# Performance work log

Hardware: AMD Instinct MI355X
Metric: run time of the kernel (lower is better)

The kernel has to match this reference:

```python
import jax, jax.numpy as jnp
import numpy as np

V, E, A, U, ENC = 10000, 512, 512, 512, 2048  # vocab, embed, attn, lstm, encoder units
B, P, S = 64, 196, 22  # batch, num_pixels, max sequence length


def setup_inputs() -> dict:
    key = jax.random.key(0)
    ks = jax.random.split(key, 16)
    init = lambda k, sh: jax.random.normal(k, sh, jnp.float32) * 0.02
    seq_lens = jax.random.randint(ks[2], (B,), 2, S + 1).at[0].set(S)  # ensure max len present
    return {
        "encoder_output": jax.random.normal(ks[0], (B, P, ENC), jnp.float32),
        "sequences": jax.random.randint(ks[1], (B, S), 0, V),
        "sequence_lengths": seq_lens,
        "emb_table": init(ks[3], (V, E)),
        "W_att_enc": init(ks[4], (ENC, A)), "b_att_enc": jnp.zeros((A,), jnp.float32),
        "W_att_gen": init(ks[5], (U, A)), "b_att_gen": jnp.zeros((A,), jnp.float32),
        "W_att_full": init(ks[6], (A, 1)), "b_att_full": jnp.zeros((1,), jnp.float32),
        "W_x": init(ks[7], (E + ENC, 4 * U)), "W_h": init(ks[8], (U, 4 * U)),
        "b_lstm": jnp.zeros((4 * U,), jnp.float32),
        "W_init_m": init(ks[9], (ENC, U)), "b_init_m": jnp.zeros((U,), jnp.float32),
        "W_init_c": init(ks[10], (ENC, U)), "b_init_c": jnp.zeros((U,), jnp.float32),
        "W_beta": init(ks[11], (U, ENC)), "b_beta": jnp.zeros((ENC,), jnp.float32),
        "W_out": init(ks[12], (U, V)), "b_out": jnp.zeros((V,), jnp.float32),
    }


def reference(encoder_output, sequences, sequence_lengths, emb_table,
              W_att_enc, b_att_enc, W_att_gen, b_att_gen, W_att_full, b_att_full,
              W_x, W_h, b_lstm, W_init_m, b_init_m, W_init_c, b_init_c,
              W_beta, b_beta, W_out, b_out):
    # Sort batch by descending caption length (as in the TF code)
    order = jnp.argsort(-sequence_lengths)
    enc = encoder_output[order]            # [B,P,ENC]
    seqs = sequences[order]                # [B,S]
    iter_lens = sequence_lengths[order] - 1  # [B]
    T = sequences.shape[1] - 1

    emb = emb_table[seqs]                  # [B,S,E]
    mean_enc = enc.mean(axis=1)            # [B,ENC]
    h = mean_enc @ W_init_m + b_init_m     # keras LSTMCell states[0] (== memory_state)
    c = mean_enc @ W_init_c + b_init_c     # keras LSTMCell states[1] (== carry_state)
    att1 = enc @ W_att_enc + b_att_enc     # [B,P,A], precomputed (constant across steps)

    def step(carry, xt):
        h, c, = carry
        emb_t, t = xt                      # emb_t: [B,E]
        mask = (t < iter_lens)[:, None]    # active rows at step t (sorted desc -> prefix)
        # attention over pixels, conditioned on carry state c
        att2 = c @ W_att_gen + b_att_gen                       # [B,A]
        e = (jax.nn.relu(att1 + att2[:, None, :]) @ W_att_full)[..., 0] + b_att_full[0]  # [B,P]
        alpha = jax.nn.softmax(e, axis=1)                      # [B,P]
        awe = jnp.einsum('bpe,bp->be', enc, alpha)             # [B,ENC]
        beta = jax.nn.sigmoid(c @ W_beta + b_beta)             # [B,ENC]
        awe = awe * beta
        # LSTM cell step (keras gate order: i, f, g, o)
        x = jnp.concatenate([emb_t, awe], axis=1)              # [B,E+ENC]
        z = x @ W_x + h @ W_h + b_lstm                         # [B,4U]
        i, f, g, o = jnp.split(z, 4, axis=1)
        c_new = jax.nn.sigmoid(f) * c + jax.nn.sigmoid(i) * jnp.tanh(g)
        h_new = jax.nn.sigmoid(o) * jnp.tanh(c_new)
        h2 = jnp.where(mask, h_new, h)
        c2 = jnp.where(mask, c_new, c)
        pred = jax.nn.softmax(c2 @ W_out + b_out, axis=1)      # prediction from carry state
        pred = jnp.where(mask, pred, 0.0)
        alpha = jnp.where(mask, alpha, 0.0)
        return (h2, c2), (pred, alpha)

    xs = (jnp.swapaxes(emb[:, :T], 0, 1), jnp.arange(T))
    _, (preds, alphas) = jax.lax.scan(step, (h, c), xs)
    predictions = jnp.swapaxes(preds, 0, 1)        # [B,T,V]
    attention_alphas = jnp.swapaxes(alphas, 0, 1)  # [B,T,P]
    return predictions, attention_alphas, seqs, iter_lens, order
```

## Files before the change

### kernel.cpp

```cpp
#include <hip/hip_runtime.h>
#include <math.h>

#define BB 64
#define PP 196
#define SS 22
#define TT 21
#define VV 10000
#define EE 512
#define AA 512
#define UU 512
#define EC 2048

#define OUT_PRED  0
#define OUT_ALPHA (BB*TT*VV)
#define OUT_SEQ   (OUT_ALPHA + BB*TT*PP)
#define OUT_ILEN  (OUT_SEQ + BB*SS)
#define OUT_ORDER (OUT_ILEN + BB)

__device__ __forceinline__ float sigm(float x) { return 1.0f / (1.0f + expf(-x)); }

__global__ void k_sort(const int* __restrict__ lens, const int* __restrict__ seqs,
                       int* __restrict__ order, int* __restrict__ ilens,
                       float* __restrict__ out)
{
    __shared__ int ord_s[BB];
    int i = threadIdx.x;
    int li = lens[i];
    int rank = 0;
    for (int j = 0; j < BB; ++j) {
        int lj = lens[j];
        rank += (lj > li) || (lj == li && j < i);
    }
    ord_s[rank] = i;
    __syncthreads();
    int o = ord_s[i];
    order[i] = o;
    int il = lens[o] - 1;
    ilens[i] = il;
    for (int s = 0; s < SS; ++s)
        out[OUT_SEQ + i * SS + s] = (float)seqs[o * SS + s];
    out[OUT_ILEN + i] = (float)il;
    out[OUT_ORDER + i] = (float)o;
}

__global__ void k_rowoff(const int* __restrict__ order, const int* __restrict__ seqs,
                         int* __restrict__ roff1, int* __restrict__ roff2)
{
    int idx = blockIdx.x * 256 + threadIdx.x;
    if (idx < BB * PP) {
        int b = idx / PP, p = idx % PP;
        roff1[idx] = order[b] * (PP * EC) + p * EC;
    }
    if (idx < BB * TT) {
        int b = idx / TT, t = idx % TT;
        int tok = seqs[order[b] * SS + t];
        roff2[idx] = tok * EE;
    }
}

__global__ __launch_bounds__(256) void k_mean(const float* __restrict__ enc,
                                              const int* __restrict__ order,
                                              float* __restrict__ meanE)
{
    int idx = blockIdx.x * 256 + threadIdx.x;
    int b = idx >> 11, e = idx & 2047;
    const float* base = enc + (size_t)order[b] * (PP * EC) + e;
    float s = 0.f;
    for (int p = 0; p < PP; ++p) s += base[p * EC];
    meanE[idx] = s * (1.0f / PP);
}

__global__ __launch_bounds__(256) void k_gemm_tile(
    const float* __restrict__ Abase, const int* __restrict__ roff,
    const float* __restrict__ W, const float* __restrict__ bias,
    float* __restrict__ C, int M, int N, int K)
{
    __shared__ float As[16][128];
    __shared__ float Bs[16][128];
    int nwg = gridDim.x, bid = blockIdx.x;
    int q = nwg >> 3, r = nwg & 7;
    int x = bid & 7, y = bid >> 3;
    int lbid = (x < r ? x * (q + 1) : r * (q + 1) + (x - r) * q) + y;
    int ntn = N >> 7;
    int mt = lbid / ntn, nt = lbid % ntn;
    int tid = threadIdx.x;

    int arow = tid >> 1, akq = (tid & 1) * 8;
    int am = mt * 128 + arow; if (am > M - 1) am = M - 1;
    const float* aptr = Abase + (size_t)roff[am] + akq;
    int bkr = tid >> 5, bc4 = (tid & 31) * 4;
    const float* bptr = W + (size_t)bkr * N + nt * 128 + bc4;

    float4 a0 = *(const float4*)(aptr);
    float4 a1 = *(const float4*)(aptr + 4);
    float4 b0 = *(const float4*)(bptr);
    float4 b1 = *(const float4*)(bptr + (size_t)8 * N);

    int tr = tid >> 4, tc = tid & 15;
    float acc[8][8] = {};

    for (int k0 = 0; k0 < K; k0 += 16) {
        float* ac = &As[akq][arow];
        ac[0]   = a0.x; ac[128] = a0.y; ac[256] = a0.z; ac[384] = a0.w;
        ac[512] = a1.x; ac[640] = a1.y; ac[768] = a1.z; ac[896] = a1.w;
        *(float4*)&Bs[bkr][bc4] = b0;
        *(float4*)&Bs[bkr + 8][bc4] = b1;
        __syncthreads();
        if (k0 + 16 < K) {
            a0 = *(const float4*)(aptr + k0 + 16);
            a1 = *(const float4*)(aptr + k0 + 20);
            b0 = *(const float4*)(bptr + (size_t)(k0 + 16) * N);
            b1 = *(const float4*)(bptr + (size_t)(k0 + 24) * N);
        }
        #pragma unroll
        for (int kk = 0; kk < 16; ++kk) {
            float4 aL = *(float4*)&As[kk][tr * 4];
            float4 aH = *(float4*)&As[kk][tr * 4 + 64];
            float4 bL = *(float4*)&Bs[kk][tc * 4];
            float4 bH = *(float4*)&Bs[kk][tc * 4 + 64];
            float av[8] = {aL.x, aL.y, aL.z, aL.w, aH.x, aH.y, aH.z, aH.w};
            float bv[8] = {bL.x, bL.y, bL.z, bL.w, bH.x, bH.y, bH.z, bH.w};
            #pragma unroll
            for (int i = 0; i < 8; ++i)
                #pragma unroll
                for (int j = 0; j < 8; ++j)
                    acc[i][j] += av[i] * bv[j];
        }
        __syncthreads();
    }
    float4 bL = make_float4(0.f, 0.f, 0.f, 0.f), bH = bL;
    if (bias) {
        bL = *(const float4*)&bias[nt * 128 + tc * 4];
        bH = *(const float4*)&bias[nt * 128 + tc * 4 + 64];
    }
    #pragma unroll
    for (int ih = 0; ih < 2; ++ih)
        #pragma unroll
        for (int i2 = 0; i2 < 4; ++i2) {
            int i = ih * 4 + i2;
            int m = mt * 128 + ih * 64 + tr * 4 + i2;
            if (m < M) {
                float4 lo, hi;
                lo.x = acc[i][0] + bL.x; lo.y = acc[i][1] + bL.y;
                lo.z = acc[i][2] + bL.z; lo.w = acc[i][3] + bL.w;
                hi.x = acc[i][4] + bH.x; hi.y = acc[i][5] + bH.y;
                hi.z = acc[i][6] + bH.z; hi.w = acc[i][7] + bH.w;
                *(float4*)&C[(size_t)m * N + nt * 128 + tc * 4] = lo;
                *(float4*)&C[(size_t)m * N + nt * 128 + tc * 4 + 64] = hi;
            }
        }
}

__global__ __launch_bounds__(256) void k_initmc(
    const float* __restrict__ meanE, const float* __restrict__ Wim,
    const float* __restrict__ bim, const float* __restrict__ Wic,
    const float* __restrict__ bic, float* __restrict__ hB, float* __restrict__ cB)
{
    __shared__ float xs[16 * 512];
    int ry = blockIdx.y, ct = blockIdx.x;
    const float* W   = blockIdx.z ? Wic : Wim;
    const float* bia = blockIdx.z ? bic : bim;
    float* out       = blockIdx.z ? cB : hB;
    int ng = threadIdx.x & 31, rg = threadIdx.x >> 5;
    int col = ct * 128 + ng * 4;
    float acc[2][4] = {};
    for (int kc = 0; kc < 4; ++kc) {
        __syncthreads();
        for (int it = 0; it < 8; ++it) {
            int i4 = (it * 256 + threadIdx.x) * 4;
            int rr = i4 >> 9, k = i4 & 511;
            *(float4*)&xs[i4] =
                *(const float4*)&meanE[(size_t)(ry * 16 + rr) * EC + kc * 512 + k];
        }
        __syncthreads();
        const float* wp = W + (size_t)(kc * 512) * 512 + col;
        #pragma unroll 8
        for (int k = 0; k < 512; ++k) {
            float4 w = *(const float4*)(wp + (size_t)k * 512);
            float x0 = xs[(rg * 2) * 512 + k], x1 = xs[(rg * 2 + 1) * 512 + k];
            acc[0][0] += x0 * w.x; acc[0][1] += x0 * w.y; acc[0][2] += x0 * w.z; acc[0][3] += x0 * w.w;
            acc[1][0] += x1 * w.x; acc[1][1] += x1 * w.y; acc[1][2] += x1 * w.z; acc[1][3] += x1 * w.w;
        }
    }
    int r0 = ry * 16 + rg * 2;
    float4 bv = *(const float4*)&bia[col];
    float4 o0, o1;
    o0.x = acc[0][0] + bv.x; o0.y = acc[0][1] + bv.y; o0.z = acc[0][2] + bv.z; o0.w = acc[0][3] + bv.w;
    o1.x = acc[1][0] + bv.x; o1.y = acc[1][1] + bv.y; o1.z = acc[1][2] + bv.z; o1.w = acc[1][3] + bv.w;
    *(float4*)&out[(size_t)r0 * 512 + col] = o0;
    *(float4*)&out[(size_t)(r0 + 1) * 512 + col] = o1;
}

__device__ __forceinline__ void mm64(
    float* __restrict__ xs,
    const float* __restrict__ x, int ldx, int kbase,
    const float* __restrict__ W, int ldw, int col0, int collim,
    float* __restrict__ dst, int ldd,
    int tcheck, const int* __restrict__ ilens)
{
    int tid = threadIdx.x;
    #pragma unroll
    for (int it = 0; it < 8; ++it) {
        int f4 = it * 256 + tid;
        int r = f4 >> 5, kf = (f4 & 31) * 4;
        *(float4*)&xs[r * 132 + kf] = *(const float4*)&x[(size_t)r * ldx + kbase + kf];
    }
    __syncthreads();
    int ng = tid & 31, rg = tid >> 5;
    int col = col0 + ng * 4;
    if (col + 4 > collim) return;
    float acc[8][4] = {};
    const float* wp = W + (size_t)kbase * ldw + col;
    #pragma unroll 4
    for (int k = 0; k < 128; ++k) {
        float4 w = *(const float4*)(wp + (size_t)k * ldw);
        #pragma unroll
        for (int i = 0; i < 8; ++i) {
            float xv = xs[(rg * 8 + i) * 132 + k];
            acc[i][0] += xv * w.x; acc[i][1] += xv * w.y;
            acc[i][2] += xv * w.z; acc[i][3] += xv * w.w;
        }
    }
    #pragma unroll
    for (int i = 0; i < 8; ++i) {
        int r = rg * 8 + i;
        if (tcheck < ilens[r])
            *(float4*)&dst[(size_t)r * ldd + col] = *(float4*)&acc[i][0];
    }
}

__device__ __forceinline__ void ab_part(
    float* xs, int b2, const float* cB, const float* Wag, const float* Wb,
    float* att2P, float* betaP, int tcheck, const int* ilens)
{
    int ct = b2 >> 2, kz = b2 & 3;
    if (ct < 4)
        mm64(xs, cB, 512, kz * 128, Wag, 512, ct * 128, 1 << 30,
             att2P + (size_t)kz * (BB * AA), 512, tcheck, ilens);
    else
        mm64(xs, cB, 512, kz * 128, Wb, 2048, (ct - 4) * 128, 1 << 30,
             betaP + (size_t)kz * (BB * EC), 2048, tcheck, ilens);
}

__global__ __launch_bounds__(256) void k_ab0(
    const float* __restrict__ cB, const float* __restrict__ Wag,
    const float* __restrict__ Wb, float* __restrict__ att2P,
    float* __restrict__ betaP, const int* __restrict__ ilens)
{
    __shared__ float xs[64 * 132];
    ab_part(xs, blockIdx.x, cB, Wag, Wb, att2P, betaP, 0, ilens);
}

__global__ __launch_bounds__(256) void k_fused1(
    const float* __restrict__ cB, const float* __restrict__ Wo,
    const float* __restrict__ Wag, const float* __restrict__ Wb,
    float* __restrict__ logitP, float* __restrict__ att2P,
    float* __restrict__ betaP, const int* __restrict__ ilens, int t)
{
    __shared__ float xs[64 * 132];
    int bid = blockIdx.x;
    if (bid < 316) {
        int ct = bid >> 2, kz = bid & 3;
        mm64(xs, cB, 512, kz * 128, Wo, VV, ct * 128, VV,
             logitP + (size_t)kz * (BB * VV), VV, t, ilens);
    } else if (t + 1 < TT) {
        ab_part(xs, bid - 316, cB, Wag, Wb, att2P, betaP, t + 1, ilens);
    }
}

__global__ __launch_bounds__(256) void k_zg(
    const float* __restrict__ aweB, const float* __restrict__ hB,
    const float* __restrict__ Wx2, const float* __restrict__ Wh,
    float* __restrict__ zP, const int* __restrict__ ilens, int t)
{
    __shared__ float xs[64 * 132];
    int ct = blockIdx.x, kz = blockIdx.y;
    if (kz < 16)
        mm64(xs, aweB, 2048, kz * 128, Wx2, 2048, ct * 128, 1 << 30,
             zP + (size_t)kz * (BB * EC), 2048, t, ilens);
    else
        mm64(xs, hB, 512, (kz - 16) * 128, Wh, 2048, ct * 128, 1 << 30,
             zP + (size_t)kz * (BB * EC), 2048, t, ilens);
}

__global__ __launch_bounds__(512) void k_scorepred(
    const float* __restrict__ att1, const float* __restrict__ att2P,
    const float* __restrict__ bgen, const float* __restrict__ Wf,
    const float* __restrict__ logitP, const float* __restrict__ bout,
    const int* __restrict__ ilens, float* __restrict__ alphaS,
    float* __restrict__ out, int t)
{
    int tid = threadIdx.x;
    if (blockIdx.x < 64) {
        int b = blockIdx.x;
        if (t >= TT || t >= ilens[b]) return;
        __shared__ float att2g[AA], wfs[AA], es[PP], red[512];
        att2g[tid] = att2P[b * AA + tid] + att2P[BB * AA + b * AA + tid]
                   + att2P[2 * BB * AA + b * AA + tid] + att2P[3 * BB * AA + b * AA + tid]
                   + bgen[tid];
        wfs[tid] = Wf[tid];
        __syncthreads();
        int wv = tid >> 6, lane = tid & 63;
        int a0 = lane * 8;
        float4 g0 = *(float4*)&att2g[a0], g1 = *(float4*)&att2g[a0 + 4];
        float4 w0 = *(float4*)&wfs[a0],  w1 = *(float4*)&wfs[a0 + 4];
        for (int p = wv; p < PP; p += 8) {
            const float4* A1 = (const float4*)(att1 + ((size_t)b * PP + p) * AA + a0);
            float4 x0 = A1[0], x1 = A1[1];
            float acc = fmaxf(x0.x + g0.x, 0.f) * w0.x + fmaxf(x0.y + g0.y, 0.f) * w0.y
                      + fmaxf(x0.z + g0.z, 0.f) * w0.z + fmaxf(x0.w + g0.w, 0.f) * w0.w
                      + fmaxf(x1.x + g1.x, 0.f) * w1.x + fmaxf(x1.y + g1.y, 0.f) * w1.y
                      + fmaxf(x1.z + g1.z, 0.f) * w1.z + fmaxf(x1.w + g1.w, 0.f) * w1.w;
            #pragma unroll
            for (int s = 32; s; s >>= 1) acc += __shfl_down(acc, s);
            if (lane == 0) es[p] = acc;
        }
        __syncthreads();
        float ev = (tid < PP) ? es[tid] : -1e30f;
        red[tid] = ev; __syncthreads();
        for (int s = 256; s >= 1; s >>= 1) {
            if (tid < s) red[tid] = fmaxf(red[tid], red[tid + s]);
            __syncthreads();
        }
        float mx = red[0]; __syncthreads();
        float ex = (tid < PP) ? expf(ev - mx) : 0.f;
        red[tid] = ex; __syncthreads();
        for (int s = 256; s >= 1; s >>= 1) {
            if (tid < s) red[tid] += red[tid + s];
            __syncthreads();
        }
        float inv = 1.0f / red[0];
        if (tid < PP) {
            float al = ex * inv;
            alphaS[b * PP + tid] = al;
            out[OUT_ALPHA + ((size_t)b * TT + t) * PP + tid] = al;
        }
    } else {
        int b = blockIdx.x - 64;
        int tp = t - 1;
        if (tp < 0 || tp >= ilens[b]) return;
        __shared__ float red8[8];
        int lane = tid & 63, wv = tid >> 6;
        const float* lb = logitP + (size_t)b * VV;
        float v[20];
        #pragma unroll
        for (int i = 0; i < 20; ++i) {
            int idx = tid + i * 512;
            if (idx < VV) {
                v[i] = lb[idx] + lb[BB * VV + idx] + lb[2 * BB * VV + idx]
                     + lb[3 * BB * VV + idx] + bout[idx];
            } else v[i] = -1e30f;
        }
        float mx = v[0];
        #pragma unroll
        for (int i = 1; i < 20; ++i) mx = fmaxf(mx, v[i]);
        #pragma unroll
        for (int s = 32; s; s >>= 1) mx = fmaxf(mx, __shfl_xor(mx, s));
        if (lane == 0) red8[wv] = mx;
        __syncthreads();
        if (tid == 0) {
            float m2 = red8[0];
            for (int i = 1; i < 8; ++i) m2 = fmaxf(m2, red8[i]);
            red8[0] = m2;
        }
        __syncthreads();
        mx = red8[0];
        __syncthreads();
        float sm = 0.f;
        #pragma unroll
        for (int i = 0; i < 20; ++i) {
            int idx = tid + i * 512;
            float e = (idx < VV) ? expf(v[i] - mx) : 0.f;
            v[i] = e; sm += e;
        }
        #pragma unroll
        for (int s = 32; s; s >>= 1) sm += __shfl_xor(sm, s);
        if (lane == 0) red8[wv] = sm;
        __syncthreads();
        if (tid == 0) {
            float s2 = 0.f;
            for (int i = 0; i < 8; ++i) s2 += red8[i];
            red8[0] = s2;
        }
        __syncthreads();
        float inv = 1.0f / red8[0];
        float* po = out + OUT_PRED + ((size_t)b * TT + tp) * VV;
        #pragma unroll
        for (int i = 0; i < 20; ++i) {
            int idx = tid + i * 512;
            if (idx < VV) po[idx] = v[i] * inv;
        }
    }
}

__global__ __launch_bounds__(256) void k_awe(
    const float* __restrict__ alphaS, const float* __restrict__ enc,
    const int* __restrict__ order, const int* __restrict__ ilens,
    const float* __restrict__ betaP, const float* __restrict__ bbeta,
    float* __restrict__ awe, int t)
{
    int b = blockIdx.y;
    if (t >= ilens[b]) return;
    int chunk = blockIdx.x, tid = threadIdx.x;
    __shared__ float al[PP];
    if (tid < PP) al[tid] = alphaS[b * PP + tid];
    __syncthreads();
    int e = chunk * 256 + tid;
    const float* ebase = enc + (size_t)order[b] * (PP * EC) + e;
    float s = 0.f;
    #pragma unroll 4
    for (int p = 0; p < PP; ++p) s += al[p] * ebase[(size_t)p * EC];
    float br = bbeta[e] + betaP[b * EC + e] + betaP[BB * EC + b * EC + e]
             + betaP[2 * BB * EC + b * EC + e] + betaP[3 * BB * EC + b * EC + e];
    awe[b * EC + e] = s * sigm(br);
}

__global__ __launch_bounds__(256) void k_gates(
    const float* __restrict__ zP, const float* __restrict__ zemb,
    const float* __restrict__ blstm, float* __restrict__ h, float* __restrict__ c,
    const int* __restrict__ ilens, int t)
{
    int idx = blockIdx.x * 256 + threadIdx.x;
    int b = idx >> 9, u = idx & 511;
    if (t >= ilens[b]) return;
    const float* ze = zemb + ((size_t)b * TT + t) * EC;
    float g[4];
    #pragma unroll
    for (int j = 0; j < 4; ++j) {
        float s = ze[u + j * 512] + blstm[u + j * 512];
        #pragma unroll
        for (int kc = 0; kc < 20; ++kc)
            s += zP[(size_t)kc * (BB * EC) + b * EC + u + j * 512];
        g[j] = s;
    }
    float cold = c[idx];
    float cn = sigm(g[1]) * cold + sigm(g[0]) * tanhf(g[2]);
    float hn = sigm(g[3]) * tanhf(cn);
    c[idx] = cn; h[idx] = hn;
}

extern "C" void kernel_launch(void* const* d_in, const int* in_sizes, int n_in,
                              void* d_out, int out_size, void* d_ws, size_t ws_size,
                              hipStream_t stream)
{
    (void)in_sizes; (void)n_in; (void)out_size; (void)ws_size;
    const float* enc  = (const float*)d_in[0];
    const int*   seqs = (const int*)d_in[1];
    const int*   lens = (const int*)d_in[2];
    const float* embT = (const float*)d_in[3];
    const float* W_ae = (const float*)d_in[4];
    const float* b_ae = (const float*)d_in[5];
    const float* W_ag = (const float*)d_in[6];
    const float* b_ag = (const float*)d_in[7];
    const float* W_af = (const float*)d_in[8];
    const float* W_x  = (const float*)d_in[10];
    const float* W_h  = (const float*)d_in[11];
    const float* b_l  = (const float*)d_in[12];
    const float* W_im = (const float*)d_in[13];
    const float* b_im = (const float*)d_in[14];
    const float* W_ic = (const float*)d_in[15];
    const float* b_ic = (const float*)d_in[16];
    const float* W_b  = (const float*)d_in[17];
    const float* b_b  = (const float*)d_in[18];
    const float* W_o  = (const float*)d_in[19];
    const float* b_o  = (const float*)d_in[20];
    float* out = (float*)d_out;

    float* ws     = (float*)d_ws;
    float* att1   = ws;
    float* zemb   = att1 + 6422528;
    float* alphaS = zemb + 2752512;
    float* aweB   = alphaS + 12544;
    float* att2P  = aweB + 131072;
    float* betaP  = att2P + 131072;
    float* hB     = betaP + 524288;
    float* cB     = hB + 32768;
    float* zlP    = cB + 32768;
    int* order = (int*)(zlP + 2621440);
    int* ilens = order + 64;
    int* roff1 = ilens + 64;
    int* roff2 = roff1 + 12544;
    float* meanE  = att2P;
    float* zP     = zlP;
    float* logitP = zlP;

    hipMemsetAsync(out, 0, (size_t)OUT_SEQ * 4, stream);

    k_sort<<<1, 64, 0, stream>>>(lens, seqs, order, ilens, out);
    k_rowoff<<<49, 256, 0, stream>>>(order, seqs, roff1, roff2);
    k_mean<<<512, 256, 0, stream>>>(enc, order, meanE);
    k_initmc<<<dim3(4, 4, 2), 256, 0, stream>>>(meanE, W_im, b_im, W_ic, b_ic, hB, cB);

    k_gemm_tile<<<98 * 4, 256, 0, stream>>>(enc, roff1, W_ae, b_ae, att1, 12544, 512, 2048);
    k_gemm_tile<<<11 * 16, 256, 0, stream>>>(embT, roff2, W_x, nullptr, zemb, 1344, 2048, 512);

    k_ab0<<<80, 256, 0, stream>>>(cB, W_ag, W_b, att2P, betaP, ilens);

    const float* Wx2 = W_x + (size_t)512 * 2048;
    for (int t = 0; t < TT; ++t) {
        k_scorepred<<<128, 512, 0, stream>>>(
            att1, att2P, b_ag, W_af, logitP, b_o, ilens, alphaS, out, t);
        k_awe<<<dim3(8, 64), 256, 0, stream>>>(
            alphaS, enc, order, ilens, betaP, b_b, aweB, t);
        k_zg<<<dim3(16, 20), 256, 0, stream>>>(aweB, hB, Wx2, W_h, zP, ilens, t);
        k_gates<<<128, 256, 0, stream>>>(zP, zemb, b_l, hB, cB, ilens, t);
        k_fused1<<<396, 256, 0, stream>>>(
            cB, W_o, W_ag, W_b, logitP, att2P, betaP, ilens, t);
    }
    k_scorepred<<<128, 512, 0, stream>>>(
        att1, att2P, b_ag, W_af, logitP, b_o, ilens, alphaS, out, TT);
}
```

Measured before the change: 2.616 ms.

## Fuse per-timestep decoder kernels into one persistent kernel with grid barriers

```diff
diff --git a/kernel.cpp b/kernel.cpp
--- a/kernel.cpp
+++ b/kernel.cpp
@@ -10,6 +10,7 @@
 #define AA 512
 #define UU 512
 #define EC 2048
+#define NBLK 512u
 
 #define OUT_PRED  0
 #define OUT_ALPHA (BB*TT*VV)
@@ -191,7 +192,27 @@
     *(float4*)&out[(size_t)(r0 + 1) * 512 + col] = o1;
 }
 
-__device__ __forceinline__ void mm64(
+__device__ __forceinline__ void gridbar(unsigned* __restrict__ bar,
+                                        unsigned* __restrict__ gen)
+{
+    __syncthreads();
+    if (threadIdx.x == 0) {
+        __threadfence();
+        unsigned g = atomicAdd(gen, 0u);
+        if (atomicAdd(bar, 1u) == NBLK - 1u) {
+            atomicExch(bar, 0u);
+            atomicAdd(gen, 1u);
+        } else {
+            unsigned spins = 0;
+            while (atomicAdd(gen, 0u) == g && ++spins < (1u << 22))
+                __builtin_amdgcn_s_sleep(1);
+        }
+        __threadfence();
+    }
+    __syncthreads();
+}
+
+__device__ __forceinline__ void mm64p(
     float* __restrict__ xs,
     const float* __restrict__ x, int ldx, int kbase,
     const float* __restrict__ W, int ldw, int col0, int collim,
@@ -208,25 +229,27 @@
     __syncthreads();
     int ng = tid & 31, rg = tid >> 5;
     int col = col0 + ng * 4;
-    if (col + 4 > collim) return;
-    float acc[8][4] = {};
-    const float* wp = W + (size_t)kbase * ldw + col;
-    #pragma unroll 4
-    for (int k = 0; k < 128; ++k) {
-        float4 w = *(const float4*)(wp + (size_t)k * ldw);
+    if (col + 4 <= collim) {
+        float acc[8][4] = {};
+        const float* wp = W + (size_t)kbase * ldw + col;
+        #pragma unroll 4
+        for (int k = 0; k < 128; ++k) {
+            float4 w = *(const float4*)(wp + (size_t)k * ldw);
+            #pragma unroll
+            for (int i = 0; i < 8; ++i) {
+                float xv = xs[(rg * 8 + i) * 132 + k];
+                acc[i][0] += xv * w.x; acc[i][1] += xv * w.y;
+                acc[i][2] += xv * w.z; acc[i][3] += xv * w.w;
+            }
+        }
         #pragma unroll
         for (int i = 0; i < 8; ++i) {
-            float xv = xs[(rg * 8 + i) * 132 + k];
-            acc[i][0] += xv * w.x; acc[i][1] += xv * w.y;
-            acc[i][2] += xv * w.z; acc[i][3] += xv * w.w;
-        }
-    }
-    #pragma unroll
-    for (int i = 0; i < 8; ++i) {
-        int r = rg * 8 + i;
-        if (tcheck < ilens[r])
-            *(float4*)&dst[(size_t)r * ldd + col] = *(float4*)&acc[i][0];
-    }
+            int r = rg * 8 + i;
+            if (tcheck < ilens[r])
+                *(float4*)&dst[(size_t)r * ldd + col] = *(float4*)&acc[i][0];
+        }
+    }
+    __syncthreads();
 }
 
 __device__ __forceinline__ void ab_part(
@@ -235,208 +258,230 @@
 {
     int ct = b2 >> 2, kz = b2 & 3;
     if (ct < 4)
-        mm64(xs, cB, 512, kz * 128, Wag, 512, ct * 128, 1 << 30,
-             att2P + (size_t)kz * (BB * AA), 512, tcheck, ilens);
+        mm64p(xs, cB, 512, kz * 128, Wag, 512, ct * 128, 1 << 30,
+              att2P + (size_t)kz * (BB * AA), 512, tcheck, ilens);
     else
-        mm64(xs, cB, 512, kz * 128, Wb, 2048, (ct - 4) * 128, 1 << 30,
-             betaP + (size_t)kz * (BB * EC), 2048, tcheck, ilens);
-}
-
-__global__ __launch_bounds__(256) void k_ab0(
-    const float* __restrict__ cB, const float* __restrict__ Wag,
-    const float* __restrict__ Wb, float* __restrict__ att2P,
-    float* __restrict__ betaP, const int* __restrict__ ilens)
-{
-    __shared__ float xs[64 * 132];
-    ab_part(xs, blockIdx.x, cB, Wag, Wb, att2P, betaP, 0, ilens);
-}
-
-__global__ __launch_bounds__(256) void k_fused1(
-    const float* __restrict__ cB, const float* __restrict__ Wo,
-    const float* __restrict__ Wag, const float* __restrict__ Wb,
-    float* __restrict__ logitP, float* __restrict__ att2P,
-    float* __restrict__ betaP, const int* __restrict__ ilens, int t)
-{
-    __shared__ float xs[64 * 132];
+        mm64p(xs, cB, 512, kz * 128, Wb, 2048, (ct - 4) * 128, 1 << 30,
+              betaP + (size_t)kz * (BB * EC), 2048, tcheck, ilens);
+}
+
+__device__ void score_part(
+    float* smem, int b, const float* __restrict__ att1,
+    const float* __restrict__ att2P, const float* __restrict__ bgen,
+    const float* __restrict__ Wf, const int* __restrict__ ilens,
+    float* __restrict__ alphaS, float* __restrict__ out, int t)
+{
+    if (t >= ilens[b]) return;
+    float* att2g = smem;
+    float* wfs   = smem + 512;
+    float* es    = smem + 1024;
+    float* red   = smem + 1232;
+    int tid = threadIdx.x;
+    for (int i = tid; i < AA; i += 256) {
+        float s = bgen[i];
+        #pragma unroll
+        for (int kz = 0; kz < 4; ++kz) s += att2P[(size_t)kz * BB * AA + b * AA + i];
+        att2g[i] = s;
+        wfs[i] = Wf[i];
+    }
+    __syncthreads();
+    int wv = tid >> 6, lane = tid & 63, a0 = lane * 8;
+    float4 g0 = *(float4*)&att2g[a0], g1 = *(float4*)&att2g[a0 + 4];
+    float4 w0 = *(float4*)&wfs[a0],  w1 = *(float4*)&wfs[a0 + 4];
+    for (int p = wv; p < PP; p += 4) {
+        const float4* A1 = (const float4*)(att1 + ((size_t)b * PP + p) * AA + a0);
+        float4 x0 = A1[0], x1 = A1[1];
+        float acc = fmaxf(x0.x + g0.x, 0.f) * w0.x + fmaxf(x0.y + g0.y, 0.f) * w0.y
+                  + fmaxf(x0.z + g0.z, 0.f) * w0.z + fmaxf(x0.w + g0.w, 0.f) * w0.w
+                  + fmaxf(x1.x + g1.x, 0.f) * w1.x + fmaxf(x1.y + g1.y, 0.f) * w1.y
+                  + fmaxf(x1.z + g1.z, 0.f) * w1.z + fmaxf(x1.w + g1.w, 0.f) * w1.w;
+        #pragma unroll
+        for (int s = 32; s; s >>= 1) acc += __shfl_down(acc, s);
+        if (lane == 0) es[p] = acc;
+    }
+    __syncthreads();
+    float ev = (tid < PP) ? es[tid] : -1e30f;
+    red[tid] = ev; __syncthreads();
+    for (int s = 128; s >= 1; s >>= 1) {
+        if (tid < s) red[tid] = fmaxf(red[tid], red[tid + s]);
+        __syncthreads();
+    }
+    float mx = red[0]; __syncthreads();
+    float ex = (tid < PP) ? expf(ev - mx) : 0.f;
+    red[tid] = ex; __syncthreads();
+    for (int s = 128; s >= 1; s >>= 1) {
+        if (tid < s) red[tid] += red[tid + s];
+        __syncthreads();
+    }
+    float inv = 1.0f / red[0];
+    if (tid < PP) {
+        float a = ex * inv;
+        alphaS[b * PP + tid] = a;
+        out[OUT_ALPHA + ((size_t)b * TT + t) * PP + tid] = a;
+    }
+}
+
+__device__ void awe_part(
+    float* smem, int bid, const float* __restrict__ alphaS,
+    const float* __restrict__ enc, const int* __restrict__ order,
+    const int* __restrict__ ilens, const float* __restrict__ betaP,
+    const float* __restrict__ bbeta, float* __restrict__ aweB, int t)
+{
+    int b = bid >> 2, chunk = bid & 3;
+    if (t >= ilens[b]) return;
+    float* al = smem;
+    int tid = threadIdx.x;
+    if (tid < PP) al[tid] = alphaS[b * PP + tid];
+    __syncthreads();
+    int o = order[b];
+    const float* ebase = enc + (size_t)o * PP * EC + chunk * 512;
+    #pragma unroll
+    for (int half = 0; half < 2; ++half) {
+        int e = half * 256 + tid;
+        float s = 0.f;
+        #pragma unroll 4
+        for (int p = 0; p < PP; ++p) s += al[p] * ebase[(size_t)p * EC + e];
+        int eg = chunk * 512 + e;
+        float br = bbeta[eg];
+        #pragma unroll
+        for (int kz = 0; kz < 4; ++kz)
+            br += betaP[(size_t)kz * BB * EC + b * EC + eg];
+        aweB[(size_t)b * EC + eg] = s * sigm(br);
+    }
+}
+
+__device__ void pred_part(
+    float* smem, int b, int tp, const float* __restrict__ logitP,
+    const float* __restrict__ bout, const int* __restrict__ ilens,
+    float* __restrict__ out)
+{
+    if (tp < 0 || tp >= ilens[b]) return;
+    float* red = smem;
+    int tid = threadIdx.x, lane = tid & 63, wv = tid >> 6;
+    const float* lb = logitP + (size_t)b * VV;
+    float* po = out + OUT_PRED + ((size_t)b * TT + tp) * VV;
+    float mx = -1e30f;
+    for (int idx = tid; idx < VV; idx += 256) {
+        float l = lb[idx] + lb[BB * VV + idx] + lb[2 * BB * VV + idx]
+                + lb[3 * BB * VV + idx] + bout[idx];
+        po[idx] = l;
+        mx = fmaxf(mx, l);
+    }
+    #pragma unroll
+    for (int s = 32; s; s >>= 1) mx = fmaxf(mx, __shfl_xor(mx, s));
+    if (lane == 0) red[wv] = mx;
+    __syncthreads();
+    mx = fmaxf(fmaxf(red[0], red[1]), fmaxf(red[2], red[3]));
+    __syncthreads();
+    float sm = 0.f;
+    for (int idx = tid; idx < VV; idx += 256) {
+        float e = expf(po[idx] - mx);
+        po[idx] = e;
+        sm += e;
+    }
+    #pragma unroll
+    for (int s = 32; s; s >>= 1) sm += __shfl_xor(sm, s);
+    if (lane == 0) red[wv] = sm;
+    __syncthreads();
+    float inv = 1.0f / (red[0] + red[1] + red[2] + red[3]);
+    for (int idx = tid; idx < VV; idx += 256) po[idx] *= inv;
+}
+
+__device__ __forceinline__ void gates_part(
+    int bid, const float* __restrict__ zlP, const float* __restrict__ zhP,
+    const float* __restrict__ zemb, const float* __restrict__ blstm,
+    float* __restrict__ h, float* __restrict__ c,
+    const int* __restrict__ ilens, int t)
+{
+    int idx = bid * 256 + threadIdx.x;
+    int b = idx >> 9, u = idx & 511;
+    if (t < ilens[b]) {
+        const float* ze = zemb + ((size_t)b * TT + t) * EC;
+        float g[4];
+        #pragma unroll
+        for (int j = 0; j < 4; ++j) {
+            float s = ze[u + j * 512] + blstm[u + j * 512];
+            #pragma unroll
+            for (int kc = 0; kc < 16; ++kc)
+                s += zlP[(size_t)kc * (BB * EC) + b * EC + u + j * 512];
+            #pragma unroll
+            for (int kc = 0; kc < 4; ++kc)
+                s += zhP[(size_t)kc * (BB * EC) + b * EC + u + j * 512];
+            g[j] = s;
+        }
+        float cold = c[idx];
+        float cn = sigm(g[1]) * cold + sigm(g[0]) * tanhf(g[2]);
+        float hn = sigm(g[3]) * tanhf(cn);
+        c[idx] = cn; h[idx] = hn;
+    }
+}
+
+__global__ __launch_bounds__(256, 2) void k_megaloop(
+    const float* __restrict__ att1, const float* __restrict__ enc,
+    const int* __restrict__ order, const int* __restrict__ ilens,
+    const float* __restrict__ bgen, const float* __restrict__ Wf,
+    const float* __restrict__ bbeta, const float* __restrict__ Wag,
+    const float* __restrict__ Wb, const float* __restrict__ Wo,
+    const float* __restrict__ Wx2, const float* __restrict__ Wh,
+    const float* __restrict__ zemb, const float* __restrict__ blstm,
+    const float* __restrict__ bout, float* __restrict__ alphaS,
+    float* __restrict__ att2P, float* __restrict__ betaP,
+    float* __restrict__ aweB, float* __restrict__ hB, float* __restrict__ cB,
+    float* __restrict__ zlP, float* __restrict__ zhP,
+    unsigned* __restrict__ bar, unsigned* __restrict__ gen,
+    float* __restrict__ out)
+{
+    __shared__ float smem[8448];
     int bid = blockIdx.x;
-    if (bid < 316) {
-        int ct = bid >> 2, kz = bid & 3;
-        mm64(xs, cB, 512, kz * 128, Wo, VV, ct * 128, VV,
-             logitP + (size_t)kz * (BB * VV), VV, t, ilens);
-    } else if (t + 1 < TT) {
-        ab_part(xs, bid - 316, cB, Wag, Wb, att2P, betaP, t + 1, ilens);
-    }
-}
-
-__global__ __launch_bounds__(256) void k_zg(
-    const float* __restrict__ aweB, const float* __restrict__ hB,
-    const float* __restrict__ Wx2, const float* __restrict__ Wh,
-    float* __restrict__ zP, const int* __restrict__ ilens, int t)
-{
-    __shared__ float xs[64 * 132];
-    int ct = blockIdx.x, kz = blockIdx.y;
-    if (kz < 16)
-        mm64(xs, aweB, 2048, kz * 128, Wx2, 2048, ct * 128, 1 << 30,
-             zP + (size_t)kz * (BB * EC), 2048, t, ilens);
-    else
-        mm64(xs, hB, 512, (kz - 16) * 128, Wh, 2048, ct * 128, 1 << 30,
-             zP + (size_t)kz * (BB * EC), 2048, t, ilens);
-}
-
-__global__ __launch_bounds__(512) void k_scorepred(
-    const float* __restrict__ att1, const float* __restrict__ att2P,
-    const float* __restrict__ bgen, const float* __restrict__ Wf,
-    const float* __restrict__ logitP, const float* __restrict__ bout,
-    const int* __restrict__ ilens, float* __restrict__ alphaS,
-    float* __restrict__ out, int t)
-{
-    int tid = threadIdx.x;
-    if (blockIdx.x < 64) {
-        int b = blockIdx.x;
-        if (t >= TT || t >= ilens[b]) return;
-        __shared__ float att2g[AA], wfs[AA], es[PP], red[512];
-        att2g[tid] = att2P[b * AA + tid] + att2P[BB * AA + b * AA + tid]
-                   + att2P[2 * BB * AA + b * AA + tid] + att2P[3 * BB * AA + b * AA + tid]
-                   + bgen[tid];
-        wfs[tid] = Wf[tid];
-        __syncthreads();
-        int wv = tid >> 6, lane = tid & 63;
-        int a0 = lane * 8;
-        float4 g0 = *(float4*)&att2g[a0], g1 = *(float4*)&att2g[a0 + 4];
-        float4 w0 = *(float4*)&wfs[a0],  w1 = *(float4*)&wfs[a0 + 4];
-        for (int p = wv; p < PP; p += 8) {
-            const float4* A1 = (const float4*)(att1 + ((size_t)b * PP + p) * AA + a0);
-            float4 x0 = A1[0], x1 = A1[1];
-            float acc = fmaxf(x0.x + g0.x, 0.f) * w0.x + fmaxf(x0.y + g0.y, 0.f) * w0.y
-                      + fmaxf(x0.z + g0.z, 0.f) * w0.z + fmaxf(x0.w + g0.w, 0.f) * w0.w
-                      + fmaxf(x1.x + g1.x, 0.f) * w1.x + fmaxf(x1.y + g1.y, 0.f) * w1.y
-                      + fmaxf(x1.z + g1.z, 0.f) * w1.z + fmaxf(x1.w + g1.w, 0.f) * w1.w;
-            #pragma unroll
-            for (int s = 32; s; s >>= 1) acc += __shfl_down(acc, s);
-            if (lane == 0) es[p] = acc;
-        }
-        __syncthreads();
-        float ev = (tid < PP) ? es[tid] : -1e30f;
-        red[tid] = ev; __syncthreads();
-        for (int s = 256; s >= 1; s >>= 1) {
-            if (tid < s) red[tid] = fmaxf(red[tid], red[tid + s]);
-            __syncthreads();
-        }
-        float mx = red[0]; __syncthreads();
-        float ex = (tid < PP) ? expf(ev - mx) : 0.f;
-        red[tid] = ex; __syncthreads();
-        for (int s = 256; s >= 1; s >>= 1) {
-            if (tid < s) red[tid] += red[tid + s];
-            __syncthreads();
-        }
-        float inv = 1.0f / red[0];
-        if (tid < PP) {
-            float al = ex * inv;
-            alphaS[b * PP + tid] = al;
-            out[OUT_ALPHA + ((size_t)b * TT + t) * PP + tid] = al;
-        }
-    } else {
-        int b = blockIdx.x - 64;
-        int tp = t - 1;
-        if (tp < 0 || tp >= ilens[b]) return;
-        __shared__ float red8[8];
-        int lane = tid & 63, wv = tid >> 6;
-        const float* lb = logitP + (size_t)b * VV;
-        float v[20];
-        #pragma unroll
-        for (int i = 0; i < 20; ++i) {
-            int idx = tid + i * 512;
-            if (idx < VV) {
-                v[i] = lb[idx] + lb[BB * VV + idx] + lb[2 * BB * VV + idx]
-                     + lb[3 * BB * VV + idx] + bout[idx];
-            } else v[i] = -1e30f;
-        }
-        float mx = v[0];
-        #pragma unroll
-        for (int i = 1; i < 20; ++i) mx = fmaxf(mx, v[i]);
-        #pragma unroll
-        for (int s = 32; s; s >>= 1) mx = fmaxf(mx, __shfl_xor(mx, s));
-        if (lane == 0) red8[wv] = mx;
-        __syncthreads();
-        if (tid == 0) {
-            float m2 = red8[0];
-            for (int i = 1; i < 8; ++i) m2 = fmaxf(m2, red8[i]);
-            red8[0] = m2;
-        }
-        __syncthreads();
-        mx = red8[0];
-        __syncthreads();
-        float sm = 0.f;
-        #pragma unroll
-        for (int i = 0; i < 20; ++i) {
-            int idx = tid + i * 512;
-            float e = (idx < VV) ? expf(v[i] - mx) : 0.f;
-            v[i] = e; sm += e;
-        }
-        #pragma unroll
-        for (int s = 32; s; s >>= 1) sm += __shfl_xor(sm, s);
-        if (lane == 0) red8[wv] = sm;
-        __syncthreads();
-        if (tid == 0) {
-            float s2 = 0.f;
-            for (int i = 0; i < 8; ++i) s2 += red8[i];
-            red8[0] = s2;
-        }
-        __syncthreads();
-        float inv = 1.0f / red8[0];
-        float* po = out + OUT_PRED + ((size_t)b * TT + tp) * VV;
-        #pragma unroll
-        for (int i = 0; i < 20; ++i) {
-            int idx = tid + i * 512;
-            if (idx < VV) po[idx] = v[i] * inv;
-        }
-    }
-}
-
-__global__ __launch_bounds__(256) void k_awe(
-    const float* __restrict__ alphaS, const float* __restrict__ enc,
-    const int* __restrict__ order, const int* __restrict__ ilens,
-    const float* __restrict__ betaP, const float* __restrict__ bbeta,
-    float* __restrict__ awe, int t)
-{
-    int b = blockIdx.y;
-    if (t >= ilens[b]) return;
-    int chunk = blockIdx.x, tid = threadIdx.x;
-    __shared__ float al[PP];
-    if (tid < PP) al[tid] = alphaS[b * PP + tid];
-    __syncthreads();
-    int e = chunk * 256 + tid;
-    const float* ebase = enc + (size_t)order[b] * (PP * EC) + e;
-    float s = 0.f;
-    #pragma unroll 4
-    for (int p = 0; p < PP; ++p) s += al[p] * ebase[(size_t)p * EC];
-    float br = bbeta[e] + betaP[b * EC + e] + betaP[BB * EC + b * EC + e]
-             + betaP[2 * BB * EC + b * EC + e] + betaP[3 * BB * EC + b * EC + e];
-    awe[b * EC + e] = s * sigm(br);
-}
-
-__global__ __launch_bounds__(256) void k_gates(
-    const float* __restrict__ zP, const float* __restrict__ zemb,
-    const float* __restrict__ blstm, float* __restrict__ h, float* __restrict__ c,
-    const int* __restrict__ ilens, int t)
-{
-    int idx = blockIdx.x * 256 + threadIdx.x;
-    int b = idx >> 9, u = idx & 511;
-    if (t >= ilens[b]) return;
-    const float* ze = zemb + ((size_t)b * TT + t) * EC;
-    float g[4];
-    #pragma unroll
-    for (int j = 0; j < 4; ++j) {
-        float s = ze[u + j * 512] + blstm[u + j * 512];
-        #pragma unroll
-        for (int kc = 0; kc < 20; ++kc)
-            s += zP[(size_t)kc * (BB * EC) + b * EC + u + j * 512];
-        g[j] = s;
-    }
-    float cold = c[idx];
-    float cn = sigm(g[1]) * cold + sigm(g[0]) * tanhf(g[2]);
-    float hn = sigm(g[3]) * tanhf(cn);
-    c[idx] = cn; h[idx] = hn;
+
+    if (bid < 80) {
+        ab_part(smem, bid, cB, Wag, Wb, att2P, betaP, 0, ilens);
+    } else if (bid < 144) {
+        int b2 = bid - 80, ct = b2 >> 2, kz = b2 & 3;
+        mm64p(smem, hB, 512, kz * 128, Wh, 2048, ct * 128, 1 << 30,
+              zhP + (size_t)kz * (BB * EC), 2048, 0, ilens);
+    }
+    gridbar(bar, gen);
+
+    for (int t = 0; t <= TT; ++t) {
+        if (t < TT) {
+            if (bid < 64)
+                score_part(smem, bid, att1, att2P, bgen, Wf, ilens, alphaS, out, t);
+            gridbar(bar, gen);
+        }
+        if (bid < 256) {
+            if (t < TT)
+                awe_part(smem, bid, alphaS, enc, order, ilens, betaP, bbeta, aweB, t);
+        } else if (bid < 320) {
+            pred_part(smem, bid - 256, t - 1, zlP, bout, ilens, out);
+        }
+        if (t == TT) break;
+        gridbar(bar, gen);
+
+        if (bid < 256) {
+            int ct = bid >> 4, kz = bid & 15;
+            mm64p(smem, aweB, 2048, kz * 128, Wx2, 2048, ct * 128, 1 << 30,
+                  zlP + (size_t)kz * (BB * EC), 2048, t, ilens);
+        }
+        gridbar(bar, gen);
+
+        if (bid < 128) gates_part(bid, zlP, zhP, zemb, blstm, hB, cB, ilens, t);
+        gridbar(bar, gen);
+
+        if (bid < 316) {
+            int ct = bid >> 2, kz = bid & 3;
+            mm64p(smem, cB, 512, kz * 128, Wo, VV, ct * 128, VV,
+                  zlP + (size_t)kz * (BB * VV), VV, t, ilens);
+        } else if (bid < 396) {
+            if (t + 1 < TT)
+                ab_part(smem, bid - 316, cB, Wag, Wb, att2P, betaP, t + 1, ilens);
+        } else if (bid < 460) {
+            int b2 = bid - 396, ct = b2 >> 2, kz = b2 & 3;
+            mm64p(smem, hB, 512, kz * 128, Wh, 2048, ct * 128, 1 << 30,
+                  zhP + (size_t)kz * (BB * EC), 2048, t + 1, ilens);
+        }
+        gridbar(bar, gen);
+    }
 }
 
 extern "C" void kernel_launch(void* const* d_in, const int* in_sizes, int n_in,
@@ -476,15 +521,17 @@
     float* hB     = betaP + 524288;
     float* cB     = hB + 32768;
     float* zlP    = cB + 32768;
-    int* order = (int*)(zlP + 2621440);
+    float* zhP    = zlP + 2560000;
+    unsigned* bar = (unsigned*)(zhP + 524288);
+    unsigned* gen = bar + 32;
+    int* order = (int*)(bar + 64);
     int* ilens = order + 64;
     int* roff1 = ilens + 64;
     int* roff2 = roff1 + 12544;
-    float* meanE  = att2P;
-    float* zP     = zlP;
-    float* logitP = zlP;
+    float* meanE = att2P;
 
     hipMemsetAsync(out, 0, (size_t)OUT_SEQ * 4, stream);
+    hipMemsetAsync(bar, 0, 256, stream);
 
     k_sort<<<1, 64, 0, stream>>>(lens, seqs, order, ilens, out);
     k_rowoff<<<49, 256, 0, stream>>>(order, seqs, roff1, roff2);
@@ -494,19 +541,9 @@
     k_gemm_tile<<<98 * 4, 256, 0, stream>>>(enc, roff1, W_ae, b_ae, att1, 12544, 512, 2048);
     k_gemm_tile<<<11 * 16, 256, 0, stream>>>(embT, roff2, W_x, nullptr, zemb, 1344, 2048, 512);
 
-    k_ab0<<<80, 256, 0, stream>>>(cB, W_ag, W_b, att2P, betaP, ilens);
-
     const float* Wx2 = W_x + (size_t)512 * 2048;
-    for (int t = 0; t < TT; ++t) {
-        k_scorepred<<<128, 512, 0, stream>>>(
-            att1, att2P, b_ag, W_af, logitP, b_o, ilens, alphaS, out, t);
-        k_awe<<<dim3(8, 64), 256, 0, stream>>>(
-            alphaS, enc, order, ilens, betaP, b_b, aweB, t);
-        k_zg<<<dim3(16, 20), 256, 0, stream>>>(aweB, hB, Wx2, W_h, zP, ilens, t);
-        k_gates<<<128, 256, 0, stream>>>(zP, zemb, b_l, hB, cB, ilens, t);
-        k_fused1<<<396, 256, 0, stream>>>(
-            cB, W_o, W_ag, W_b, logitP, att2P, betaP, ilens, t);
-    }
-    k_scorepred<<<128, 512, 0, stream>>>(
-        att1, att2P, b_ag, W_af, logitP, b_o, ilens, alphaS, out, TT);
-}
+    k_megaloop<<<NBLK, 256, 0, stream>>>(
+        att1, enc, order, ilens, b_ag, W_af, b_b, W_ag, W_b, W_o, Wx2, W_h,
+        zemb, b_l, b_o, alphaS, att2P, betaP, aweB, hB, cB, zlP, zhP,
+        bar, gen, out);
+}
```

After: 8.153 ms. 212% more time.

## Move h@W_h into previous step's fused kernel and shrink precompute GEMM tiles

Applied to the files above, without the earlier changes.

```diff
diff --git a/kernel.cpp b/kernel.cpp
--- a/kernel.cpp
+++ b/kernel.cpp
@@ -70,12 +70,12 @@
     meanE[idx] = s * (1.0f / PP);
 }
 
-__global__ __launch_bounds__(256) void k_gemm_tile(
+__global__ __launch_bounds__(256) void k_gemm_tile64(
     const float* __restrict__ Abase, const int* __restrict__ roff,
     const float* __restrict__ W, const float* __restrict__ bias,
     float* __restrict__ C, int M, int N, int K)
 {
-    __shared__ float As[16][128];
+    __shared__ float As[16][72];
     __shared__ float Bs[16][128];
     int nwg = gridDim.x, bid = blockIdx.x;
     int q = nwg >> 3, r = nwg & 7;
@@ -85,70 +85,56 @@
     int mt = lbid / ntn, nt = lbid % ntn;
     int tid = threadIdx.x;
 
-    int arow = tid >> 1, akq = (tid & 1) * 8;
-    int am = mt * 128 + arow; if (am > M - 1) am = M - 1;
-    const float* aptr = Abase + (size_t)roff[am] + akq;
+    int arow = tid & 63, ak4 = (tid >> 6) * 4;
+    int am = mt * 64 + arow; if (am > M - 1) am = M - 1;
+    const float* aptr = Abase + (size_t)roff[am] + ak4;
     int bkr = tid >> 5, bc4 = (tid & 31) * 4;
     const float* bptr = W + (size_t)bkr * N + nt * 128 + bc4;
 
     float4 a0 = *(const float4*)(aptr);
-    float4 a1 = *(const float4*)(aptr + 4);
     float4 b0 = *(const float4*)(bptr);
     float4 b1 = *(const float4*)(bptr + (size_t)8 * N);
 
-    int tr = tid >> 4, tc = tid & 15;
-    float acc[8][8] = {};
+    int tr = tid >> 5, tc = tid & 31;
+    float acc[8][4] = {};
 
     for (int k0 = 0; k0 < K; k0 += 16) {
-        float* ac = &As[akq][arow];
-        ac[0]   = a0.x; ac[128] = a0.y; ac[256] = a0.z; ac[384] = a0.w;
-        ac[512] = a1.x; ac[640] = a1.y; ac[768] = a1.z; ac[896] = a1.w;
+        float* ac = &As[ak4][arow];
+        ac[0] = a0.x; ac[72] = a0.y; ac[144] = a0.z; ac[216] = a0.w;
         *(float4*)&Bs[bkr][bc4] = b0;
         *(float4*)&Bs[bkr + 8][bc4] = b1;
         __syncthreads();
         if (k0 + 16 < K) {
             a0 = *(const float4*)(aptr + k0 + 16);
-            a1 = *(const float4*)(aptr + k0 + 20);
             b0 = *(const float4*)(bptr + (size_t)(k0 + 16) * N);
             b1 = *(const float4*)(bptr + (size_t)(k0 + 24) * N);
         }
         #pragma unroll
         for (int kk = 0; kk < 16; ++kk) {
-            float4 aL = *(float4*)&As[kk][tr * 4];
-            float4 aH = *(float4*)&As[kk][tr * 4 + 64];
-            float4 bL = *(float4*)&Bs[kk][tc * 4];
-            float4 bH = *(float4*)&Bs[kk][tc * 4 + 64];
+            float4 aL = *(float4*)&As[kk][tr * 8];
+            float4 aH = *(float4*)&As[kk][tr * 8 + 4];
+            float4 bb = *(float4*)&Bs[kk][tc * 4];
             float av[8] = {aL.x, aL.y, aL.z, aL.w, aH.x, aH.y, aH.z, aH.w};
-            float bv[8] = {bL.x, bL.y, bL.z, bL.w, bH.x, bH.y, bH.z, bH.w};
             #pragma unroll
-            for (int i = 0; i < 8; ++i)
-                #pragma unroll
-                for (int j = 0; j < 8; ++j)
-                    acc[i][j] += av[i] * bv[j];
-        }
-        __syncthreads();
-    }
-    float4 bL = make_float4(0.f, 0.f, 0.f, 0.f), bH = bL;
-    if (bias) {
-        bL = *(const float4*)&bias[nt * 128 + tc * 4];
-        bH = *(const float4*)&bias[nt * 128 + tc * 4 + 64];
-    }
+            for (int i = 0; i < 8; ++i) {
+                acc[i][0] += av[i] * bb.x; acc[i][1] += av[i] * bb.y;
+                acc[i][2] += av[i] * bb.z; acc[i][3] += av[i] * bb.w;
+            }
+        }
+        __syncthreads();
+    }
+    float4 bv = make_float4(0.f, 0.f, 0.f, 0.f);
+    if (bias) bv = *(const float4*)&bias[nt * 128 + tc * 4];
     #pragma unroll
-    for (int ih = 0; ih < 2; ++ih)
-        #pragma unroll
-        for (int i2 = 0; i2 < 4; ++i2) {
-            int i = ih * 4 + i2;
-            int m = mt * 128 + ih * 64 + tr * 4 + i2;
-            if (m < M) {
-                float4 lo, hi;
-                lo.x = acc[i][0] + bL.x; lo.y = acc[i][1] + bL.y;
-                lo.z = acc[i][2] + bL.z; lo.w = acc[i][3] + bL.w;
-                hi.x = acc[i][4] + bH.x; hi.y = acc[i][5] + bH.y;
-                hi.z = acc[i][6] + bH.z; hi.w = acc[i][7] + bH.w;
-                *(float4*)&C[(size_t)m * N + nt * 128 + tc * 4] = lo;
-                *(float4*)&C[(size_t)m * N + nt * 128 + tc * 4 + 64] = hi;
-            }
-        }
+    for (int i = 0; i < 8; ++i) {
+        int m = mt * 64 + tr * 8 + i;
+        if (m < M) {
+            float4 rr;
+            rr.x = acc[i][0] + bv.x; rr.y = acc[i][1] + bv.y;
+            rr.z = acc[i][2] + bv.z; rr.w = acc[i][3] + bv.w;
+            *(float4*)&C[(size_t)m * N + nt * 128 + tc * 4] = rr;
+        }
+    }
 }
 
 __global__ __launch_bounds__(256) void k_initmc(
@@ -242,20 +228,35 @@
              betaP + (size_t)kz * (BB * EC), 2048, tcheck, ilens);
 }
 
-__global__ __launch_bounds__(256) void k_ab0(
-    const float* __restrict__ cB, const float* __restrict__ Wag,
-    const float* __restrict__ Wb, float* __restrict__ att2P,
-    float* __restrict__ betaP, const int* __restrict__ ilens)
+__device__ __forceinline__ void zh_part(
+    float* xs, int b2, const float* hB, const float* Wh,
+    float* zhP, int tcheck, const int* ilens)
+{
+    int ct = b2 >> 2, kz = b2 & 3;
+    mm64(xs, hB, 512, kz * 128, Wh, 2048, ct * 128, 1 << 30,
+         zhP + (size_t)kz * (BB * EC), 2048, tcheck, ilens);
+}
+
+__global__ __launch_bounds__(256) void k_pre(
+    const float* __restrict__ cB, const float* __restrict__ hB,
+    const float* __restrict__ Wag, const float* __restrict__ Wb,
+    const float* __restrict__ Wh, float* __restrict__ att2P,
+    float* __restrict__ betaP, float* __restrict__ zhP,
+    const int* __restrict__ ilens)
 {
     __shared__ float xs[64 * 132];
-    ab_part(xs, blockIdx.x, cB, Wag, Wb, att2P, betaP, 0, ilens);
+    int bid = blockIdx.x;
+    if (bid < 80) ab_part(xs, bid, cB, Wag, Wb, att2P, betaP, 0, ilens);
+    else          zh_part(xs, bid - 80, hB, Wh, zhP, 0, ilens);
 }
 
 __global__ __launch_bounds__(256) void k_fused1(
-    const float* __restrict__ cB, const float* __restrict__ Wo,
-    const float* __restrict__ Wag, const float* __restrict__ Wb,
+    const float* __restrict__ cB, const float* __restrict__ hB,
+    const float* __restrict__ Wo, const float* __restrict__ Wag,
+    const float* __restrict__ Wb, const float* __restrict__ Wh,
     float* __restrict__ logitP, float* __restrict__ att2P,
-    float* __restrict__ betaP, const int* __restrict__ ilens, int t)
+    float* __restrict__ betaP, float* __restrict__ zhP,
+    const int* __restrict__ ilens, int t)
 {
     __shared__ float xs[64 * 132];
     int bid = blockIdx.x;
@@ -263,24 +264,23 @@
         int ct = bid >> 2, kz = bid & 3;
         mm64(xs, cB, 512, kz * 128, Wo, VV, ct * 128, VV,
              logitP + (size_t)kz * (BB * VV), VV, t, ilens);
-    } else if (t + 1 < TT) {
-        ab_part(xs, bid - 316, cB, Wag, Wb, att2P, betaP, t + 1, ilens);
+    } else if (bid < 396) {
+        if (t + 1 < TT)
+            ab_part(xs, bid - 316, cB, Wag, Wb, att2P, betaP, t + 1, ilens);
+    } else {
+        if (t + 1 < TT)
+            zh_part(xs, bid - 396, hB, Wh, zhP, t + 1, ilens);
     }
 }
 
 __global__ __launch_bounds__(256) void k_zg(
-    const float* __restrict__ aweB, const float* __restrict__ hB,
-    const float* __restrict__ Wx2, const float* __restrict__ Wh,
-    float* __restrict__ zP, const int* __restrict__ ilens, int t)
+    const float* __restrict__ aweB, const float* __restrict__ Wx2,
+    float* __restrict__ zlP, const int* __restrict__ ilens, int t)
 {
     __shared__ float xs[64 * 132];
-    int ct = blockIdx.x, kz = blockIdx.y;
-    if (kz < 16)
-        mm64(xs, aweB, 2048, kz * 128, Wx2, 2048, ct * 128, 1 << 30,
-             zP + (size_t)kz * (BB * EC), 2048, t, ilens);
-    else
-        mm64(xs, hB, 512, (kz - 16) * 128, Wh, 2048, ct * 128, 1 << 30,
-             zP + (size_t)kz * (BB * EC), 2048, t, ilens);
+    int ct = blockIdx.x >> 4, kz = blockIdx.x & 15;
+    mm64(xs, aweB, 2048, kz * 128, Wx2, 2048, ct * 128, 1 << 30,
+         zlP + (size_t)kz * (BB * EC), 2048, t, ilens);
 }
 
 __global__ __launch_bounds__(512) void k_scorepred(
@@ -416,8 +416,9 @@
 }
 
 __global__ __launch_bounds__(256) void k_gates(
-    const float* __restrict__ zP, const float* __restrict__ zemb,
-    const float* __restrict__ blstm, float* __restrict__ h, float* __restrict__ c,
+    const float* __restrict__ zlP, const float* __restrict__ zhP,
+    const float* __restrict__ zemb, const float* __restrict__ blstm,
+    float* __restrict__ h, float* __restrict__ c,
     const int* __restrict__ ilens, int t)
 {
     int idx = blockIdx.x * 256 + threadIdx.x;
@@ -429,8 +430,11 @@
     for (int j = 0; j < 4; ++j) {
         float s = ze[u + j * 512] + blstm[u + j * 512];
         #pragma unroll
-        for (int kc = 0; kc < 20; ++kc)
-            s += zP[(size_t)kc * (BB * EC) + b * EC + u + j * 512];
+        for (int kc = 0; kc < 16; ++kc)
+            s += zlP[(size_t)kc * (BB * EC) + b * EC + u + j * 512];
+        #pragma unroll
+        for (int kc = 0; kc < 4; ++kc)
+            s += zhP[(size_t)kc * (BB * EC) + b * EC + u + j * 512];
         g[j] = s;
     }
     float cold = c[idx];
@@ -476,12 +480,12 @@
     float* hB     = betaP + 524288;
     float* cB     = hB + 32768;
     float* zlP    = cB + 32768;
-    int* order = (int*)(zlP + 2621440);
+    float* zhP    = zlP + 2560000;
+    int* order = (int*)(zhP + 524288);
     int* ilens = order + 64;
     int* roff1 = ilens + 64;
     int* roff2 = roff1 + 12544;
     float* meanE  = att2P;
-    float* zP     = zlP;
     float* logitP = zlP;
 
     hipMemsetAsync(out, 0, (size_t)OUT_SEQ * 4, stream);
@@ -491,10 +495,10 @@
     k_mean<<<512, 256, 0, stream>>>(enc, order, meanE);
     k_initmc<<<dim3(4, 4, 2), 256, 0, stream>>>(meanE, W_im, b_im, W_ic, b_ic, hB, cB);
 
-    k_gemm_tile<<<98 * 4, 256, 0, stream>>>(enc, roff1, W_ae, b_ae, att1, 12544, 512, 2048);
-    k_gemm_tile<<<11 * 16, 256, 0, stream>>>(embT, roff2, W_x, nullptr, zemb, 1344, 2048, 512);
-
-    k_ab0<<<80, 256, 0, stream>>>(cB, W_ag, W_b, att2P, betaP, ilens);
+    k_gemm_tile64<<<196 * 4, 256, 0, stream>>>(enc, roff1, W_ae, b_ae, att1, 12544, 512, 2048);
+    k_gemm_tile64<<<21 * 16, 256, 0, stream>>>(embT, roff2, W_x, nullptr, zemb, 1344, 2048, 512);
+
+    k_pre<<<144, 256, 0, stream>>>(cB, hB, W_ag, W_b, W_h, att2P, betaP, zhP, ilens);
 
     const float* Wx2 = W_x + (size_t)512 * 2048;
     for (int t = 0; t < TT; ++t) {
@@ -502,10 +506,10 @@
             att1, att2P, b_ag, W_af, logitP, b_o, ilens, alphaS, out, t);
         k_awe<<<dim3(8, 64), 256, 0, stream>>>(
             alphaS, enc, order, ilens, betaP, b_b, aweB, t);
-        k_zg<<<dim3(16, 20), 256, 0, stream>>>(aweB, hB, Wx2, W_h, zP, ilens, t);
-        k_gates<<<128, 256, 0, stream>>>(zP, zemb, b_l, hB, cB, ilens, t);
-        k_fused1<<<396, 256, 0, stream>>>(
-            cB, W_o, W_ag, W_b, logitP, att2P, betaP, ilens, t);
+        k_zg<<<256, 256, 0, stream>>>(aweB, Wx2, zlP, ilens, t);
+        k_gates<<<128, 256, 0, stream>>>(zlP, zhP, zemb, b_l, hB, cB, ilens, t);
+        k_fused1<<<460, 256, 0, stream>>>(
+            cB, hB, W_o, W_ag, W_b, W_h, logitP, att2P, betaP, zhP, ilens, t);
     }
     k_scorepred<<<128, 512, 0, stream>>>(
         att1, att2P, b_ag, W_af, logitP, b_o, ilens, alphaS, out, TT);
```

After: 2.678 ms. 1.02x slower.
